# Kernel tuning notes

Hardware: AMD Instinct MI355X
Metric: run time of the kernel (lower is better)

## Reference

```python
import jax, jax.numpy as jnp
import numpy as np

D_MODEL = 1024
NUM_HEADS = 16
D_K = D_MODEL // NUM_HEADS
THETA = 10000.0


def setup_inputs() -> dict:
    key = jax.random.key(0)
    ks = jax.random.split(key, 5)
    B, S = 2, 2048
    sigma = np.sqrt(2.0 / (D_MODEL + D_MODEL))
    x = jax.random.normal(ks[0], (B, S, D_MODEL), dtype=jnp.float32)
    Wq = jax.random.normal(ks[1], (D_MODEL, D_MODEL), dtype=jnp.float32) * sigma
    Wk = jax.random.normal(ks[2], (D_MODEL, D_MODEL), dtype=jnp.float32) * sigma
    Wv = jax.random.normal(ks[3], (D_MODEL, D_MODEL), dtype=jnp.float32) * sigma
    Wo = jax.random.normal(ks[4], (D_MODEL, D_MODEL), dtype=jnp.float32) * sigma
    return {"x": x, "Wq": Wq, "Wk": Wk, "Wv": Wv, "Wo": Wo}


def _rope(x, cos, sin):
    # x: [B, H, S, D_K]; cos/sin: [S, D_K//2] broadcast to [1, 1, S, D_K//2]
    x1 = x[..., ::2]
    x2 = x[..., 1::2]
    even = x1 * cos - x2 * sin
    odd = x1 * sin + x2 * cos
    return jnp.stack((even, odd), axis=-1).reshape(x.shape)


def reference(x, Wq, Wk, Wv, Wo):
    B, S, _ = x.shape
    # projections: weight is (out, in), applied as einsum('oi,...i->...o')
    q = jnp.einsum('oi,bsi->bso', Wq, x).reshape(B, S, NUM_HEADS, D_K).transpose(0, 2, 1, 3)
    k = jnp.einsum('oi,bsi->bso', Wk, x).reshape(B, S, NUM_HEADS, D_K).transpose(0, 2, 1, 3)
    v = jnp.einsum('oi,bsi->bso', Wv, x).reshape(B, S, NUM_HEADS, D_K).transpose(0, 2, 1, 3)
    # RoPE tables (token_positions = arange(S))
    inv_freq = 1.0 / (THETA ** (jnp.arange(0, D_K, 2, dtype=jnp.float32) / D_K))
    t = jnp.arange(S, dtype=jnp.float32)
    freqs = t[:, None] * inv_freq[None, :]          # [S, D_K/2]
    cos = jnp.cos(freqs)[None, None]                # [1,1,S,D_K/2]
    sin = jnp.sin(freqs)[None, None]
    q = _rope(q, cos, sin)
    k = _rope(k, cos, sin)
    # causal attention, full materialized scores (faithful to source)
    scores = jnp.einsum('bhid,bhjd->bhij', q, k) / np.sqrt(D_K).astype(np.float32)
    causal = jnp.tril(jnp.ones((S, S), dtype=bool))
    scores = jnp.where(causal, scores, -jnp.inf)
    attn = jax.nn.softmax(scores, axis=-1)
    out = jnp.einsum('bhij,bhjd->bhid', attn, v)    # [B,H,S,D_K]
    out = out.transpose(0, 2, 1, 3).reshape(B, S, D_MODEL)
    return jnp.einsum('oi,bsi->bso', Wo, out)
```

## Files before the change

### kernel.cpp

```cpp
#include <hip/hip_runtime.h>

#define D_MODEL 1024
#define NUM_HEADS 16
#define SEQ 2048
#define BATCH 2

typedef __attribute__((ext_vector_type(8))) short bf16x8;
typedef __attribute__((ext_vector_type(4))) float f32x4;

__device__ __forceinline__ float bf2f(unsigned short u) {
    return __uint_as_float(((unsigned int)u) << 16);
}
__device__ __forceinline__ unsigned short f2bf(float f) {
    unsigned int u = __float_as_uint(f);
    return (unsigned short)((u + 0x7FFFu + ((u >> 16) & 1u)) >> 16);
}
__device__ __forceinline__ ushort4 pack4(float4 v) {
    return make_ushort4(f2bf(v.x), f2bf(v.y), f2bf(v.z), f2bf(v.w));
}

__device__ __forceinline__ void gload_lds16(const unsigned short* g, unsigned short* l) {
    __builtin_amdgcn_global_load_lds(
        (const __attribute__((address_space(1))) unsigned int*)g,
        (__attribute__((address_space(3))) unsigned int*)l,
        16, 0, 0);
}

__device__ __forceinline__ bf16x8 lds_read_swz(const unsigned short (*tile)[64], int row, int chunk) {
    const char* p = reinterpret_cast<const char*>(tile);
    return *reinterpret_cast<const bf16x8*>(p + row * 128 + (((chunk ^ (row & 7))) << 4));
}

__global__ __launch_bounds__(256) void conv_kernel(
    const float* __restrict__ src, unsigned short* __restrict__ dst, int n4)
{
    int i = blockIdx.x * 256 + threadIdx.x;
    if (i < n4) {
        float4 v = reinterpret_cast<const float4*>(src)[i];
        reinterpret_cast<ushort4*>(dst)[i] = pack4(v);
    }
}

__global__ __launch_bounds__(256) void conv4_kernel(
    const float* __restrict__ x, const float* __restrict__ Wq,
    const float* __restrict__ Wk, const float* __restrict__ Wv,
    unsigned short* __restrict__ xb, unsigned short* __restrict__ w3bf)
{
    int i = blockIdx.x * 256 + threadIdx.x;
    const float* src;
    unsigned short* dst;
    int off;
    if (i < 1048576) {
        src = x; dst = xb; off = i;
    } else {
        int j = i - 1048576;
        int which = j >> 18;
        off = j & 0x3FFFF;
        src = (which == 0) ? Wq : (which == 1) ? Wk : Wv;
        dst = w3bf + ((size_t)which << 20);
        off = off;
    }
    float4 v = reinterpret_cast<const float4*>(src)[off];
    reinterpret_cast<ushort4*>(dst)[off] = pack4(v);
}

__global__ __launch_bounds__(256) void qkv_mfma_kernel(
    const unsigned short* __restrict__ xb,
    const unsigned short* __restrict__ w3,
    unsigned short* __restrict__ qb, unsigned short* __restrict__ kb,
    unsigned short* __restrict__ vt)
{
    const int lin = blockIdx.x;
    const int b = lin & 7;
    const int t = lin >> 3;
    const int which = t % 3;
    const int y = t / 3;
    const unsigned short* __restrict__ W = w3 + (size_t)which * 1048576;
    const int m0 = y * 128;
    const int n0g = b * 128;

    __shared__ __align__(16) unsigned short As[2][128][64];
    __shared__ __align__(16) unsigned short Bs[2][128][64];

    const int tid = threadIdx.x;
    const int w = tid >> 6;
    const int lane = tid & 63;
    const int quad = lane >> 4;
    const int c15 = lane & 15;
    const int qm = w >> 1, qn = w & 1;
    const int srow8 = lane >> 3;
    const int sch = lane & 7;

    auto stage = [&](int k0, int buf) {
#pragma unroll
        for (int i = 0; i < 4; i++) {
            const int row = i * 32 + w * 8 + srow8;
            const int ch = sch ^ (row & 7);
            gload_lds16(xb + (size_t)(m0 + row) * 1024 + k0 + ch * 8,
                        &As[buf][i * 32 + w * 8][0]);
            gload_lds16(W + (size_t)(n0g + row) * 1024 + k0 + ch * 8,
                        &Bs[buf][i * 32 + w * 8][0]);
        }
    };

    f32x4 acc[4][4];
#pragma unroll
    for (int mi = 0; mi < 4; mi++)
#pragma unroll
        for (int ni = 0; ni < 4; ni++) acc[mi][ni] = (f32x4){0.f, 0.f, 0.f, 0.f};

    stage(0, 0);
    for (int k0 = 0; k0 < 1024; k0 += 64) {
        const int cb = (k0 >> 6) & 1;
        __syncthreads();
        if (k0 < 960) stage(k0 + 64, cb ^ 1);

        bf16x8 af[2][4], bfr[2][4];
#pragma unroll
        for (int ks = 0; ks < 2; ks++) {
#pragma unroll
            for (int mi = 0; mi < 4; mi++)
                af[ks][mi] = lds_read_swz(As[cb], qm * 64 + mi * 16 + c15, ks * 4 + quad);
#pragma unroll
            for (int ni = 0; ni < 4; ni++)
                bfr[ks][ni] = lds_read_swz(Bs[cb], qn * 64 + ni * 16 + c15, ks * 4 + quad);
        }
#pragma unroll
        for (int ks = 0; ks < 2; ks++)
#pragma unroll
            for (int mi = 0; mi < 4; mi++)
#pragma unroll
                for (int ni = 0; ni < 4; ni++)
                    acc[mi][ni] = __builtin_amdgcn_mfma_f32_16x16x32_bf16(af[ks][mi], bfr[ks][ni], acc[mi][ni], 0, 0, 0);
    }

    __syncthreads();
    unsigned short* stg = &As[0][0][0] + w * (16 * 72);
    const int hq = b * 2 + qn;
    unsigned short* outp = (which == 0) ? qb : kb;

    float invf[4];
#pragma unroll
    for (int ni = 0; ni < 4; ni++)
        invf[ni] = powf(10000.0f, -((float)(((ni * 16 + c15) & 63) >> 1)) / 32.0f);
    const int odd = c15 & 1;

#pragma unroll
    for (int mi = 0; mi < 4; mi++) {
#pragma unroll
        for (int r = 0; r < 4; r++) {
            int m = m0 + qm * 64 + mi * 16 + quad * 4 + r;
            int s = m & (SEQ - 1);
#pragma unroll
            for (int ni = 0; ni < 4; ni++) {
                float val = acc[mi][ni][r];
                float res;
                if (which < 2) {
                    float part = __shfl_xor(val, 1);
                    float sn, cs;
                    sincosf((float)s * invf[ni], &sn, &cs);
                    res = odd ? (part * sn + val * cs) : (val * cs - part * sn);
                } else {
                    res = val;
                }
                stg[(quad * 4 + r) * 72 + ni * 16 + c15] = f2bf(res);
            }
        }
        if (which < 2) {
            int row = lane >> 2;
            int ch = lane & 3;
            int m = m0 + qm * 64 + mi * 16 + row;
            int s = m & (SEQ - 1);
            int bb = m >> 11;
            size_t ob = (((size_t)bb * NUM_HEADS + hq) * SEQ + s) * 64 + ch * 16;
            uint4 v0 = *reinterpret_cast<const uint4*>(&stg[row * 72 + ch * 16]);
            uint4 v1 = *reinterpret_cast<const uint4*>(&stg[row * 72 + ch * 16 + 8]);
            *reinterpret_cast<uint4*>(&outp[ob]) = v0;
            *reinterpret_cast<uint4*>(&outp[ob + 8]) = v1;
        } else {
            int mbase = m0 + qm * 64 + mi * 16;
            int bb = mbase >> 11;
            int s_base = mbase & (SEQ - 1);
            unsigned short tmp[16];
#pragma unroll
            for (int sl = 0; sl < 16; sl++) tmp[sl] = stg[sl * 72 + lane];
            size_t ob = (((size_t)bb * NUM_HEADS + hq) * 64 + lane) * SEQ + s_base;
            *reinterpret_cast<uint4*>(&vt[ob])     = *reinterpret_cast<uint4*>(&tmp[0]);
            *reinterpret_cast<uint4*>(&vt[ob + 8]) = *reinterpret_cast<uint4*>(&tmp[8]);
        }
    }
}

__global__ __launch_bounds__(256) void attn_kernel(
    const unsigned short* __restrict__ qb, const unsigned short* __restrict__ kb,
    const unsigned short* __restrict__ vt, unsigned short* __restrict__ ab)
{
    const int xpair = blockIdx.x;
    const int bh = blockIdx.y;
    const int b = bh >> 4, h = bh & 15;
    const size_t base = (size_t)bh * SEQ * 64;
    const size_t vbase = (size_t)bh * 64 * SEQ;
    const int tid = threadIdx.x;
    const int w = tid >> 6;
    const int lane = tid & 63;
    const int quad = lane >> 4;
    const int c15 = lane & 15;
    const int srow8 = lane >> 3;
    const int sch = lane & 7;

    __shared__ __align__(16) unsigned short Ks[2][64][64];
    __shared__ __align__(16) unsigned short Vs[2][64][64];
    __shared__ __align__(16) unsigned short Pl[64][72];

    auto stage = [&](int jts, int buf) {
        const int j0s = jts * 64;
#pragma unroll
        for (int i = 0; i < 2; i++) {
            const int row = w * 16 + i * 8 + srow8;
            const int ch = sch ^ (row & 7);
            gload_lds16(kb + base + (size_t)(j0s + row) * 64 + ch * 8,
                        &Ks[buf][w * 16 + i * 8][0]);
            gload_lds16(vt + vbase + (size_t)row * SEQ + j0s + ch * 8,
                        &Vs[buf][w * 16 + i * 8][0]);
        }
    };

    for (int pass = 0; pass < 2; pass++) {
        const int it = pass ? xpair : (31 - xpair);
        const int i0 = it * 64;

        const int qrow = i0 + w * 16 + c15;
        bf16x8 qf0 = *reinterpret_cast<const bf16x8*>(&qb[base + (size_t)qrow * 64 + quad * 8]);
        bf16x8 qf1 = *reinterpret_cast<const bf16x8*>(&qb[base + (size_t)qrow * 64 + 32 + quad * 8]);

        float m_st[4], l_st[4];
        f32x4 Oc[4];
#pragma unroll
        for (int r = 0; r < 4; r++) { m_st[r] = -1e30f; l_st[r] = 0.f; }
#pragma unroll
        for (int t = 0; t < 4; t++) Oc[t] = (f32x4){0.f, 0.f, 0.f, 0.f};

        __syncthreads();
        stage(0, 0);

        for (int jt = 0; jt <= it; jt++) {
            const int j0 = jt * 64;
            const int cb = jt & 1;

            __syncthreads();
            if (jt < it) stage(jt + 1, cb ^ 1);

            bf16x8 kc0[4], kc1[4];
#pragma unroll
            for (int t = 0; t < 4; t++) {
                kc0[t] = lds_read_swz(Ks[cb], t * 16 + c15, quad);
                kc1[t] = lds_read_swz(Ks[cb], t * 16 + c15, 4 + quad);
            }

            f32x4 sc[4];
#pragma unroll
            for (int t = 0; t < 4; t++) sc[t] = (f32x4){0.f, 0.f, 0.f, 0.f};
#pragma unroll
            for (int t = 0; t < 4; t++) {
                sc[t] = __builtin_amdgcn_mfma_f32_16x16x32_bf16(qf0, kc0[t], sc[t], 0, 0, 0);
                sc[t] = __builtin_amdgcn_mfma_f32_16x16x32_bf16(qf1, kc1[t], sc[t], 0, 0, 0);
            }

            bf16x8 vv0[4], vv1[4];
#pragma unroll
            for (int t = 0; t < 4; t++) {
                vv0[t] = lds_read_swz(Vs[cb], t * 16 + c15, quad);
                vv1[t] = lds_read_swz(Vs[cb], t * 16 + c15, 4 + quad);
            }

#pragma unroll
            for (int t = 0; t < 4; t++)
#pragma unroll
                for (int r = 0; r < 4; r++) sc[t][r] *= 0.125f;
            if (jt == it) {
#pragma unroll
                for (int t = 0; t < 4; t++) {
                    int gj = j0 + t * 16 + c15;
#pragma unroll
                    for (int r = 0; r < 4; r++) {
                        int gi = i0 + w * 16 + quad * 4 + r;
                        if (gj > gi) sc[t][r] = -1e30f;
                    }
                }
            }

            float mnew[4], alpha[4], rsum[4];
#pragma unroll
            for (int r = 0; r < 4; r++) {
                float tm = fmaxf(fmaxf(sc[0][r], sc[1][r]), fmaxf(sc[2][r], sc[3][r]));
                tm = fmaxf(tm, __shfl_xor(tm, 1));
                tm = fmaxf(tm, __shfl_xor(tm, 2));
                tm = fmaxf(tm, __shfl_xor(tm, 4));
                tm = fmaxf(tm, __shfl_xor(tm, 8));
                mnew[r] = fmaxf(m_st[r], tm);
                alpha[r] = __expf(m_st[r] - mnew[r]);
                rsum[r] = 0.f;
            }
#pragma unroll
            for (int t = 0; t < 4; t++) {
#pragma unroll
                for (int r = 0; r < 4; r++) {
                    float p = __expf(sc[t][r] - mnew[r]);
                    rsum[r] += p;
                    Pl[w * 16 + quad * 4 + r][t * 16 + c15] = f2bf(p);
                }
            }
#pragma unroll
            for (int r = 0; r < 4; r++) {
                float s = rsum[r];
                s += __shfl_xor(s, 1);
                s += __shfl_xor(s, 2);
                s += __shfl_xor(s, 4);
                s += __shfl_xor(s, 8);
                l_st[r] = l_st[r] * alpha[r] + s;
                m_st[r] = mnew[r];
#pragma unroll
                for (int t = 0; t < 4; t++) Oc[t][r] *= alpha[r];
            }

            bf16x8 ap0 = *reinterpret_cast<const bf16x8*>(&Pl[w * 16 + c15][quad * 8]);
            bf16x8 ap1 = *reinterpret_cast<const bf16x8*>(&Pl[w * 16 + c15][32 + quad * 8]);
#pragma unroll
            for (int t = 0; t < 4; t++) {
                Oc[t] = __builtin_amdgcn_mfma_f32_16x16x32_bf16(ap0, vv0[t], Oc[t], 0, 0, 0);
                Oc[t] = __builtin_amdgcn_mfma_f32_16x16x32_bf16(ap1, vv1[t], Oc[t], 0, 0, 0);
            }
        }

#pragma unroll
        for (int r = 0; r < 4; r++) {
            float inv = 1.0f / l_st[r];
#pragma unroll
            for (int t = 0; t < 4; t++)
                Pl[w * 16 + quad * 4 + r][t * 16 + c15] = f2bf(Oc[t][r] * inv);
        }
        {
            int row = lane >> 2;
            int ch = lane & 3;
            int gi = i0 + w * 16 + row;
            size_t ob = ((size_t)b * SEQ + gi) * 1024 + h * 64 + ch * 16;
            uint4 v0 = *reinterpret_cast<const uint4*>(&Pl[w * 16 + row][ch * 16]);
            uint4 v1 = *reinterpret_cast<const uint4*>(&Pl[w * 16 + row][ch * 16 + 8]);
            *reinterpret_cast<uint4*>(&ab[ob]) = v0;
            *reinterpret_cast<uint4*>(&ab[ob + 8]) = v1;
        }
    }
}

__global__ __launch_bounds__(256) void out_mfma_kernel(
    const unsigned short* __restrict__ A, const unsigned short* __restrict__ Wob,
    float* __restrict__ out)
{
    const int lin = blockIdx.x;
    const int b = lin & 7;
    const int y = lin >> 3;
    const int m0 = y * 128;
    const int n0g = b * 128;

    __shared__ __align__(16) unsigned short As[2][128][64];
    __shared__ __align__(16) unsigned short Bs[2][128][64];

    const int tid = threadIdx.x;
    const int w = tid >> 6;
    const int lane = tid & 63;
    const int quad = lane >> 4;
    const int c15 = lane & 15;
    const int qm = w >> 1, qn = w & 1;
    const int srow8 = lane >> 3;
    const int sch = lane & 7;

    auto stage = [&](int k0, int buf) {
#pragma unroll
        for (int i = 0; i < 4; i++) {
            const int row = i * 32 + w * 8 + srow8;
            const int ch = sch ^ (row & 7);
            gload_lds16(A + (size_t)(m0 + row) * 1024 + k0 + ch * 8,
                        &As[buf][i * 32 + w * 8][0]);
            gload_lds16(Wob + (size_t)(n0g + row) * 1024 + k0 + ch * 8,
                        &Bs[buf][i * 32 + w * 8][0]);
        }
    };

    f32x4 acc[4][4];
#pragma unroll
    for (int mi = 0; mi < 4; mi++)
#pragma unroll
        for (int ni = 0; ni < 4; ni++) acc[mi][ni] = (f32x4){0.f, 0.f, 0.f, 0.f};

    stage(0, 0);
    for (int k0 = 0; k0 < 1024; k0 += 64) {
        const int cb = (k0 >> 6) & 1;
        __syncthreads();
        if (k0 < 960) stage(k0 + 64, cb ^ 1);

        bf16x8 af[2][4], bfr[2][4];
#pragma unroll
        for (int ks = 0; ks < 2; ks++) {
#pragma unroll
            for (int mi = 0; mi < 4; mi++)
                af[ks][mi] = lds_read_swz(As[cb], qm * 64 + mi * 16 + c15, ks * 4 + quad);
#pragma unroll
            for (int ni = 0; ni < 4; ni++)
                bfr[ks][ni] = lds_read_swz(Bs[cb], qn * 64 + ni * 16 + c15, ks * 4 + quad);
        }
#pragma unroll
        for (int ks = 0; ks < 2; ks++)
#pragma unroll
            for (int mi = 0; mi < 4; mi++)
#pragma unroll
                for (int ni = 0; ni < 4; ni++)
                    acc[mi][ni] = __builtin_amdgcn_mfma_f32_16x16x32_bf16(af[ks][mi], bfr[ks][ni], acc[mi][ni], 0, 0, 0);
    }

#pragma unroll
    for (int mi = 0; mi < 4; mi++) {
#pragma unroll
        for (int r = 0; r < 4; r++) {
            int m = m0 + qm * 64 + mi * 16 + quad * 4 + r;
#pragma unroll
            for (int ni = 0; ni < 4; ni++) {
                int n = n0g + qn * 64 + ni * 16 + c15;
                out[(size_t)m * 1024 + n] = acc[mi][ni][r];
            }
        }
    }
}

extern "C" void kernel_launch(void* const* d_in, const int* in_sizes, int n_in,
                              void* d_out, int out_size, void* d_ws, size_t ws_size,
                              hipStream_t stream)
{
    const float* x  = (const float*)d_in[0];
    const float* Wq = (const float*)d_in[1];
    const float* Wk = (const float*)d_in[2];
    const float* Wv = (const float*)d_in[3];
    const float* Wo = (const float*)d_in[4];
    float* out = (float*)d_out;

    const size_t QKV_ELEMS = (size_t)BATCH * SEQ * D_MODEL;

    unsigned short* qb = (unsigned short*)d_ws;
    unsigned short* kb = qb + QKV_ELEMS;
    unsigned short* vt = kb + QKV_ELEMS;
    unsigned short* ab = vt + QKV_ELEMS;
    unsigned short* w3bf = ab;
    unsigned short* wobf = qb;
    unsigned short* xbuf = (unsigned short*)d_out;

    conv4_kernel<<<dim3(7168), 256, 0, stream>>>(x, Wq, Wk, Wv, xbuf, w3bf);
    qkv_mfma_kernel<<<dim3(768), 256, 0, stream>>>(xbuf, w3bf, qb, kb, vt);
    attn_kernel<<<dim3(16, 32), 256, 0, stream>>>(qb, kb, vt, ab);
    conv_kernel<<<dim3(1024), 256, 0, stream>>>(Wo, wobf, 262144);
    out_mfma_kernel<<<dim3(256), 256, 0, stream>>>(ab, wobf, out);
}
```

Measured before the change: 237.7 us.

## Transpose attention MFMAs so each lane owns one query row, with lazy rescaling

Swaps the MFMA operand order so that score and output accumulators are transposed. Each lane then holds a single query row, which means the row max and row sum need only two cross-lane shuffles, and the running max and sum become scalars instead of 4-element arrays. It folds the 1/sqrt(d) scale into an fma inside the exp and skips the rescale of the accumulator and sum whenever no lane's max grows by more than a threshold. P and the output are written to LDS as packed 32-bit pairs. The deferred-max trick trades a bounded growth of the exponent range for fewer multiplies and less divergence.

Result: faster. 218.3 us (-8.2%).

```diff
diff --git a/kernel.cpp b/kernel.cpp
--- a/kernel.cpp
+++ b/kernel.cpp
@@ -58,7 +58,6 @@
         off = j & 0x3FFFF;
         src = (which == 0) ? Wq : (which == 1) ? Wk : Wv;
         dst = w3bf + ((size_t)which << 20);
-        off = off;
     }
     float4 v = reinterpret_cast<const float4*>(src)[off];
     reinterpret_cast<ushort4*>(dst)[off] = pack4(v);
@@ -207,6 +206,7 @@
     const int c15 = lane & 15;
     const int srow8 = lane >> 3;
     const int sch = lane & 7;
+    const float C = 0.125f;
 
     __shared__ __align__(16) unsigned short Ks[2][64][64];
     __shared__ __align__(16) unsigned short Vs[2][64][64];
@@ -233,10 +233,8 @@
         bf16x8 qf0 = *reinterpret_cast<const bf16x8*>(&qb[base + (size_t)qrow * 64 + quad * 8]);
         bf16x8 qf1 = *reinterpret_cast<const bf16x8*>(&qb[base + (size_t)qrow * 64 + 32 + quad * 8]);
 
-        float m_st[4], l_st[4];
+        float m_st = -1e30f, l_st = 0.f;
         f32x4 Oc[4];
-#pragma unroll
-        for (int r = 0; r < 4; r++) { m_st[r] = -1e30f; l_st[r] = 0.f; }
 #pragma unroll
         for (int t = 0; t < 4; t++) Oc[t] = (f32x4){0.f, 0.f, 0.f, 0.f};
 
@@ -262,8 +260,8 @@
             for (int t = 0; t < 4; t++) sc[t] = (f32x4){0.f, 0.f, 0.f, 0.f};
 #pragma unroll
             for (int t = 0; t < 4; t++) {
-                sc[t] = __builtin_amdgcn_mfma_f32_16x16x32_bf16(qf0, kc0[t], sc[t], 0, 0, 0);
-                sc[t] = __builtin_amdgcn_mfma_f32_16x16x32_bf16(qf1, kc1[t], sc[t], 0, 0, 0);
+                sc[t] = __builtin_amdgcn_mfma_f32_16x16x32_bf16(kc0[t], qf0, sc[t], 0, 0, 0);
+                sc[t] = __builtin_amdgcn_mfma_f32_16x16x32_bf16(kc1[t], qf1, sc[t], 0, 0, 0);
             }
 
             bf16x8 vv0[4], vv1[4];
@@ -273,71 +271,83 @@
                 vv1[t] = lds_read_swz(Vs[cb], t * 16 + c15, 4 + quad);
             }
 
-#pragma unroll
-            for (int t = 0; t < 4; t++)
-#pragma unroll
-                for (int r = 0; r < 4; r++) sc[t][r] *= 0.125f;
             if (jt == it) {
+                const int gi = i0 + w * 16 + c15;
 #pragma unroll
                 for (int t = 0; t < 4; t++) {
-                    int gj = j0 + t * 16 + c15;
 #pragma unroll
                     for (int r = 0; r < 4; r++) {
-                        int gi = i0 + w * 16 + quad * 4 + r;
+                        int gj = j0 + t * 16 + quad * 4 + r;
                         if (gj > gi) sc[t][r] = -1e30f;
                     }
                 }
             }
 
-            float mnew[4], alpha[4], rsum[4];
-#pragma unroll
-            for (int r = 0; r < 4; r++) {
-                float tm = fmaxf(fmaxf(sc[0][r], sc[1][r]), fmaxf(sc[2][r], sc[3][r]));
-                tm = fmaxf(tm, __shfl_xor(tm, 1));
-                tm = fmaxf(tm, __shfl_xor(tm, 2));
-                tm = fmaxf(tm, __shfl_xor(tm, 4));
-                tm = fmaxf(tm, __shfl_xor(tm, 8));
-                mnew[r] = fmaxf(m_st[r], tm);
-                alpha[r] = __expf(m_st[r] - mnew[r]);
-                rsum[r] = 0.f;
-            }
+            float x0 = fmaxf(fmaxf(sc[0][0], sc[0][1]), fmaxf(sc[0][2], sc[0][3]));
+            float x1 = fmaxf(fmaxf(sc[1][0], sc[1][1]), fmaxf(sc[1][2], sc[1][3]));
+            float x2 = fmaxf(fmaxf(sc[2][0], sc[2][1]), fmaxf(sc[2][2], sc[2][3]));
+            float x3 = fmaxf(fmaxf(sc[3][0], sc[3][1]), fmaxf(sc[3][2], sc[3][3]));
+            float tm = fmaxf(fmaxf(x0, x1), fmaxf(x2, x3));
+            tm = fmaxf(tm, __shfl_xor(tm, 16));
+            tm = fmaxf(tm, __shfl_xor(tm, 32));
+
+            if (!__all(tm <= m_st + 64.0f)) {
+                float mnew = fmaxf(m_st, tm);
+                float alpha = __expf((m_st - mnew) * C);
+                l_st *= alpha;
+#pragma unroll
+                for (int t = 0; t < 4; t++)
+#pragma unroll
+                    for (int r = 0; r < 4; r++) Oc[t][r] *= alpha;
+                m_st = mnew;
+            }
+
+            const float mC = m_st * C;
+            float p[4][4];
+#pragma unroll
+            for (int t = 0; t < 4; t++)
+#pragma unroll
+                for (int r = 0; r < 4; r++)
+                    p[t][r] = __expf(__builtin_fmaf(sc[t][r], C, -mC));
+
+            float s0 = (p[0][0] + p[0][1]) + (p[0][2] + p[0][3]);
+            float s1 = (p[1][0] + p[1][1]) + (p[1][2] + p[1][3]);
+            float s2 = (p[2][0] + p[2][1]) + (p[2][2] + p[2][3]);
+            float s3 = (p[3][0] + p[3][1]) + (p[3][2] + p[3][3]);
+            l_st += (s0 + s1) + (s2 + s3);
+
 #pragma unroll
             for (int t = 0; t < 4; t++) {
 #pragma unroll
-                for (int r = 0; r < 4; r++) {
-                    float p = __expf(sc[t][r] - mnew[r]);
-                    rsum[r] += p;
-                    Pl[w * 16 + quad * 4 + r][t * 16 + c15] = f2bf(p);
+                for (int hh = 0; hh < 2; hh++) {
+                    unsigned int pk = (unsigned int)f2bf(p[t][2 * hh])
+                                    | ((unsigned int)f2bf(p[t][2 * hh + 1]) << 16);
+                    *reinterpret_cast<unsigned int*>(
+                        &Pl[w * 16 + c15][t * 16 + quad * 4 + 2 * hh]) = pk;
                 }
-            }
-#pragma unroll
-            for (int r = 0; r < 4; r++) {
-                float s = rsum[r];
-                s += __shfl_xor(s, 1);
-                s += __shfl_xor(s, 2);
-                s += __shfl_xor(s, 4);
-                s += __shfl_xor(s, 8);
-                l_st[r] = l_st[r] * alpha[r] + s;
-                m_st[r] = mnew[r];
-#pragma unroll
-                for (int t = 0; t < 4; t++) Oc[t][r] *= alpha[r];
             }
 
             bf16x8 ap0 = *reinterpret_cast<const bf16x8*>(&Pl[w * 16 + c15][quad * 8]);
             bf16x8 ap1 = *reinterpret_cast<const bf16x8*>(&Pl[w * 16 + c15][32 + quad * 8]);
 #pragma unroll
             for (int t = 0; t < 4; t++) {
-                Oc[t] = __builtin_amdgcn_mfma_f32_16x16x32_bf16(ap0, vv0[t], Oc[t], 0, 0, 0);
-                Oc[t] = __builtin_amdgcn_mfma_f32_16x16x32_bf16(ap1, vv1[t], Oc[t], 0, 0, 0);
-            }
-        }
-
-#pragma unroll
-        for (int r = 0; r < 4; r++) {
-            float inv = 1.0f / l_st[r];
-#pragma unroll
-            for (int t = 0; t < 4; t++)
-                Pl[w * 16 + quad * 4 + r][t * 16 + c15] = f2bf(Oc[t][r] * inv);
+                Oc[t] = __builtin_amdgcn_mfma_f32_16x16x32_bf16(vv0[t], ap0, Oc[t], 0, 0, 0);
+                Oc[t] = __builtin_amdgcn_mfma_f32_16x16x32_bf16(vv1[t], ap1, Oc[t], 0, 0, 0);
+            }
+        }
+
+        l_st += __shfl_xor(l_st, 16);
+        l_st += __shfl_xor(l_st, 32);
+        float inv = 1.0f / l_st;
+#pragma unroll
+        for (int t = 0; t < 4; t++) {
+#pragma unroll
+            for (int hh = 0; hh < 2; hh++) {
+                unsigned int pk = (unsigned int)f2bf(Oc[t][2 * hh] * inv)
+                                | ((unsigned int)f2bf(Oc[t][2 * hh + 1] * inv) << 16);
+                *reinterpret_cast<unsigned int*>(
+                    &Pl[w * 16 + c15][t * 16 + quad * 4 + 2 * hh]) = pk;
+            }
         }
         {
             int row = lane >> 2;
```
